# Kernel optimization log

Measured on AMD Instinct MI355X. Metric: run time of the kernel, lower is better.

The kernel has to match this reference:

```python
import jax, jax.numpy as jnp
import numpy as np

SEQ_LEN = 2048
VOCAB = 32000
EMB = 512
HID = 1024


def setup_inputs() -> dict:
    key = jax.random.key(0)
    ks = jax.random.split(key, 8)
    s = lambda n: 1.0 / np.sqrt(n)
    return {
        "tokens": jax.random.randint(ks[0], (SEQ_LEN,), 0, VOCAB, dtype=jnp.int64 if jax.config.jax_enable_x64 else jnp.int32),
        "embedding_mat": jax.random.normal(ks[1], (VOCAB, EMB), dtype=jnp.float32),
        "W1": jax.random.normal(ks[2], (EMB, HID), dtype=jnp.float32) * s(EMB),
        "U1": jax.random.normal(ks[3], (HID, HID), dtype=jnp.float32) * s(HID),
        "b1": jnp.zeros((HID,), dtype=jnp.float32),
        "W2": jax.random.normal(ks[4], (HID, EMB), dtype=jnp.float32) * s(HID),
        "U2": jax.random.normal(ks[5], (EMB, EMB), dtype=jnp.float32) * s(EMB),
        "b2": jnp.zeros((EMB,), dtype=jnp.float32),
    }


def _rnn_scan(inputs, W1, U1, b1, W2, U2, b2):
    # 2-layer vanilla tanh RNN over time; inputs: [T, EMB] -> outputs: [T, EMB]
    h1_0 = jnp.zeros((W1.shape[1],), dtype=inputs.dtype)
    h2_0 = jnp.zeros((W2.shape[1],), dtype=inputs.dtype)

    def step(carry, x_t):
        h1, h2 = carry
        h1 = jnp.tanh(x_t @ W1 + h1 @ U1 + b1)
        h2 = jnp.tanh(h1 @ W2 + h2 @ U2 + b2)
        return (h1, h2), h2

    _, outs = jax.lax.scan(step, (h1_0, h2_0), inputs)
    return outs


def reference(tokens, embedding_mat, W1, U1, b1, W2, U2, b2):
    # embed tokens, shift right by one (teacher forcing with zero BOS)
    embedded = jnp.take(embedding_mat, tokens, axis=0)          # [T, EMB]
    inputs = jnp.pad(embedded, ((1, 0), (0, 0)))[:-1]           # [T, EMB]
    rnn_outputs = _rnn_scan(inputs, W1, U1, b1, W2, U2, b2)     # [T, EMB]
    logits = rnn_outputs @ embedding_mat.T                      # [T, V]
    raw_log_probs = jax.nn.log_softmax(logits, axis=1)          # [T, V]
    log_probs = jnp.take_along_axis(raw_log_probs, tokens[:, None], axis=1)[:, 0]
    return jnp.sum(log_probs)
```

## Files before the change

### kernel.cpp

```cpp
#include <hip/hip_runtime.h>
#include <stdint.h>


#define TSEQ 2048
#define NVOCAB 32000
#define DEMB 512
#define DHID 1024
#define CAN 0xFFFFFFFFu

typedef __attribute__((ext_vector_type(8))) short short8;
typedef __attribute__((ext_vector_type(4))) float f32x4;
typedef unsigned long long u64;

__device__ __forceinline__ unsigned short f2bf(float f) {
  union { float f; unsigned u; } v; v.f = f;
  unsigned r = (v.u + 0x7FFFu + ((v.u >> 16) & 1u)) >> 16;
  return (unsigned short)r;
}

__device__ __forceinline__ f32x4 llc_ld16(const float* p) {
  f32x4 r;
  asm volatile("global_load_dwordx4 %0, %1, off sc0 sc1\n\ts_waitcnt vmcnt(0)"
               : "=&v"(r) : "v"(p) : "memory");
  return r;
}

__device__ __forceinline__ void llc_ld16x2(const float* pa, const float* pb,
                                           f32x4& a, f32x4& b) {
  asm volatile("global_load_dwordx4 %0, %2, off sc0 sc1\n\t"
               "global_load_dwordx4 %1, %3, off sc0 sc1\n\t"
               "s_waitcnt vmcnt(0)"
               : "=&v"(a), "=&v"(b) : "v"(pa), "v"(pb) : "memory");
}

__device__ __forceinline__ void llc_st16(float* p, f32x4 v) {
  asm volatile("global_store_dwordx4 %0, %1, off sc0 sc1"
               :: "v"(p), "v"(v) : "memory");
}

__device__ __forceinline__ bool okq(f32x4 v) {
  return __float_as_uint(v.x) != CAN && __float_as_uint(v.y) != CAN &&
         __float_as_uint(v.z) != CAN && __float_as_uint(v.w) != CAN;
}

__device__ __forceinline__ f32x4 rotq(f32x4 h) {
  f32x4 r;
  r.x = __int_as_float(__builtin_amdgcn_mov_dpp(__float_as_int(h.x), 0x121, 0xf, 0xf, false));
  r.y = __int_as_float(__builtin_amdgcn_mov_dpp(__float_as_int(h.y), 0x121, 0xf, 0xf, false));
  r.z = __int_as_float(__builtin_amdgcn_mov_dpp(__float_as_int(h.z), 0x121, 0xf, 0xf, false));
  r.w = __int_as_float(__builtin_amdgcn_mov_dpp(__float_as_int(h.w), 0x121, 0xf, 0xf, false));
  return r;
}

__device__ __forceinline__ float tanh_fast(float x) {
  float ax = fabsf(x);
  float e = __expf(ax + ax);
  float t = 1.f - __fdividef(2.f, e + 1.f);
  return (x < 0.f) ? -t : t;
}

__global__ void k_init(uint4* __restrict__ h1v4, uint4* __restrict__ h2v4) {
  const int n1 = (TSEQ + 1) * DHID / 4;
  const int n2 = (TSEQ + 1) * DEMB / 4;
  uint4 can; can.x = CAN; can.y = CAN; can.z = CAN; can.w = CAN;
  uint4 zer; zer.x = 0u; zer.y = 0u; zer.z = 0u; zer.w = 0u;
  const int stride = gridDim.x * blockDim.x;
  for (int i = blockIdx.x * blockDim.x + threadIdx.x; i < n1 + n2; i += stride) {
    if (i < n1) {
      h1v4[i] = (i < DHID / 4) ? zer : can;
    } else {
      int j = i - n1;
      h2v4[j] = (j < DEMB / 4) ? zer : can;
    }
  }
}

__global__ __launch_bounds__(256) void k_xw1(const int* __restrict__ tok,
                                             const float* __restrict__ emb,
                                             const float* __restrict__ W1,
                                             const float* __restrict__ b1,
                                             float* __restrict__ xW1) {
  __shared__ float in_lds[16 * DEMB];
  const int tid = threadIdx.x;
  const int rb = blockIdx.x >> 2, cb = blockIdx.x & 3;
  const int t0 = rb * 16, j0 = cb * 256;
  for (int idx = tid; idx < 16 * 128; idx += 256) {
    int r = idx >> 7, q = idx & 127;
    int t = t0 + r;
    float4 v;
    if (t == 0) { v.x = 0.f; v.y = 0.f; v.z = 0.f; v.w = 0.f; }
    else        { v = *(const float4*)(emb + (size_t)tok[t - 1] * DEMB + q * 4); }
    *(float4*)&in_lds[r * DEMB + q * 4] = v;
  }
  __syncthreads();
  const int j = j0 + tid;
  float acc[16];
  {
    float bb = b1[j];
#pragma unroll
    for (int r = 0; r < 16; ++r) acc[r] = bb;
  }
  for (int k = 0; k < DEMB; k += 4) {
    const float* wp = W1 + (size_t)k * DHID + j;
    float w0 = wp[0], w1 = wp[DHID], w2 = wp[2 * DHID], w3 = wp[3 * DHID];
#pragma unroll
    for (int r = 0; r < 16; ++r) {
      float4 h = *(const float4*)&in_lds[r * DEMB + k];
      acc[r] += h.x * w0;
      acc[r] += h.y * w1;
      acc[r] += h.z * w2;
      acc[r] += h.w * w3;
    }
  }
#pragma unroll
  for (int r = 0; r < 16; ++r) xW1[(size_t)(t0 + r) * DHID + j] = acc[r];
}

__global__ __launch_bounds__(256, 1) void k_rnn(const float* __restrict__ xW1,
                                                const float* __restrict__ U1,
                                                const float* __restrict__ W2,
                                                const float* __restrict__ U2,
                                                const float* __restrict__ b2,
                                                float* __restrict__ h1v,
                                                float* __restrict__ h2v,
                                                float* __restrict__ h2buf) {
  __shared__ float cmb[2][160];
  const int tid = threadIdx.x;
  const int wg = blockIdx.x;
  const int l = tid & 63, w = tid >> 6;
  const int r = l >> 4, i = l & 15;

  if (wg < 32) {
    const int c0 = wg * 32;
    float wA[64], wB[64];
#pragma unroll
    for (int j = 0; j < 16; ++j) {
      int sl = (i - j) & 15;
      const float* up = U1 + (size_t)(256 * w + 64 * r + 4 * sl) * DHID + c0;
#pragma unroll
      for (int e = 0; e < 4; ++e) {
        wA[4 * j + e] = up[(size_t)e * DHID + i];
        wB[4 * j + e] = up[(size_t)e * DHID + i + 16];
      }
    }
    for (int st = 0; st < TSEQ; ++st) {
      float xv = 0.f;
      if (w == 0) xv = xW1[(size_t)st * DHID + c0 + (l & 31)];
      f32x4 h;
      {
        const float* sp = h1v + (size_t)st * DHID + 4 * tid;
        while (true) { h = llc_ld16(sp); if (okq(h)) break; }
      }
      float a0 = 0.f, a1 = 0.f;
#pragma unroll
      for (int j = 0; j < 16; ++j) {
        a0 += h.x * wA[4 * j + 0]; a1 += h.x * wB[4 * j + 0];
        a0 += h.y * wA[4 * j + 1]; a1 += h.y * wB[4 * j + 1];
        a0 += h.z * wA[4 * j + 2]; a1 += h.z * wB[4 * j + 2];
        a0 += h.w * wA[4 * j + 3]; a1 += h.w * wB[4 * j + 3];
        if (j < 15) h = rotq(h);
      }
      a0 += __shfl_xor(a0, 16); a0 += __shfl_xor(a0, 32);
      a1 += __shfl_xor(a1, 16); a1 += __shfl_xor(a1, 32);
      const int par = st & 1;
      if (l < 16) {
        cmb[par][i * 5 + w] = a0;
        cmb[par][(i + 16) * 5 + w] = a1;
      }
      __syncthreads();
      if (w == 0) {
        const float* cp = &cmb[par][(l & 31) * 5];
        float s4 = (cp[0] + cp[1]) + (cp[2] + cp[3]);
        float hv = tanh_fast(xv + s4);
        float g1 = __shfl_down(hv, 1);
        float g2 = __shfl_down(hv, 2);
        float g3 = __shfl_down(hv, 3);
        if (l < 32 && (l & 3) == 0) {
          f32x4 o; o.x = hv; o.y = g1; o.z = g2; o.w = g3;
          llc_st16(h1v + (size_t)(st + 1) * DHID + c0 + l, o);
        }
      }
    }
  } else {
    const int c0 = (wg - 32) * 32;
    float qAA[64], qAB[64], qBA[64], qBB[64];
#pragma unroll
    for (int j = 0; j < 16; ++j) {
      int sl = (i - j) & 15;
      const float* mp = W2 + (size_t)(256 * w + 64 * r + 4 * sl) * DEMB + c0;
#pragma unroll
      for (int e = 0; e < 4; ++e) {
        qAA[4 * j + e] = mp[(size_t)e * DEMB + i];
        qAB[4 * j + e] = mp[(size_t)e * DEMB + i + 16];
      }
    }
    if (w < 2) {
#pragma unroll
      for (int j = 0; j < 16; ++j) {
        int sl = (i - j) & 15;
        const float* mp = U2 + (size_t)(256 * w + 64 * r + 4 * sl) * DEMB + c0;
#pragma unroll
        for (int e = 0; e < 4; ++e) {
          qBA[4 * j + e] = mp[(size_t)e * DEMB + i];
          qBB[4 * j + e] = mp[(size_t)e * DEMB + i + 16];
        }
      }
    }
    float bias = 0.f;
    if (w == 0) bias = b2[c0 + (l & 31)];
    for (int t = 0; t < TSEQ; ++t) {
      f32x4 hA, hB;
      const float* spA = h1v + (size_t)(t + 1) * DHID + 4 * tid;
      if (w < 2) {
        const float* spB = h2v + (size_t)t * DEMB + 4 * tid;
        while (true) {
          f32x4 xa, xb;
          llc_ld16x2(spA, spB, xa, xb);
          if (okq(xa) && okq(xb)) { hA = xa; hB = xb; break; }
        }
      } else {
        while (true) { f32x4 xa = llc_ld16(spA); if (okq(xa)) { hA = xa; break; } }
      }
      float a0 = 0.f, a1 = 0.f;
#pragma unroll
      for (int j = 0; j < 16; ++j) {
        a0 += hA.x * qAA[4 * j + 0]; a1 += hA.x * qAB[4 * j + 0];
        a0 += hA.y * qAA[4 * j + 1]; a1 += hA.y * qAB[4 * j + 1];
        a0 += hA.z * qAA[4 * j + 2]; a1 += hA.z * qAB[4 * j + 2];
        a0 += hA.w * qAA[4 * j + 3]; a1 += hA.w * qAB[4 * j + 3];
        if (j < 15) hA = rotq(hA);
      }
      if (w < 2) {
#pragma unroll
        for (int j = 0; j < 16; ++j) {
          a0 += hB.x * qBA[4 * j + 0]; a1 += hB.x * qBB[4 * j + 0];
          a0 += hB.y * qBA[4 * j + 1]; a1 += hB.y * qBB[4 * j + 1];
          a0 += hB.z * qBA[4 * j + 2]; a1 += hB.z * qBB[4 * j + 2];
          a0 += hB.w * qBA[4 * j + 3]; a1 += hB.w * qBB[4 * j + 3];
          if (j < 15) hB = rotq(hB);
        }
      }
      a0 += __shfl_xor(a0, 16); a0 += __shfl_xor(a0, 32);
      a1 += __shfl_xor(a1, 16); a1 += __shfl_xor(a1, 32);
      const int par = t & 1;
      if (l < 16) {
        cmb[par][i * 5 + w] = a0;
        cmb[par][(i + 16) * 5 + w] = a1;
      }
      __syncthreads();
      if (w == 0) {
        const float* cp = &cmb[par][(l & 31) * 5];
        float s4 = (cp[0] + cp[1]) + (cp[2] + cp[3]);
        float hv = tanh_fast(s4 + bias);
        float g1 = __shfl_down(hv, 1);
        float g2 = __shfl_down(hv, 2);
        float g3 = __shfl_down(hv, 3);
        if (l < 32 && (l & 3) == 0) {
          f32x4 o; o.x = hv; o.y = g1; o.z = g2; o.w = g3;
          llc_st16(h2v + (size_t)(t + 1) * DEMB + c0 + l, o);
          *(f32x4*)(h2buf + (size_t)(t + 1) * DEMB + c0 + l) = o;
        }
      }
    }
  }
}

__global__ void k_conv(const float* __restrict__ emb, const float* __restrict__ h2f,
                       unsigned short* __restrict__ embB, unsigned short* __restrict__ h2b) {
  const int n1 = NVOCAB * DEMB / 4;
  const int n2 = TSEQ * DEMB / 4;
  const int stride = gridDim.x * blockDim.x;
  for (int i = blockIdx.x * blockDim.x + threadIdx.x; i < n1 + n2; i += stride) {
    float4 v;
    if (i < n1) v = ((const float4*)emb)[i];
    else        v = ((const float4*)h2f)[i - n1];
    ushort4 o;
    o.x = f2bf(v.x); o.y = f2bf(v.y); o.z = f2bf(v.z); o.w = f2bf(v.w);
    if (i < n1) ((ushort4*)embB)[i] = o;
    else        ((ushort4*)h2b)[i - n1] = o;
  }
}

__global__ __launch_bounds__(256, 1) void k_logits(const unsigned short* __restrict__ Ab,
                                                   const unsigned short* __restrict__ Bb,
                                                   float* __restrict__ pmax,
                                                   float* __restrict__ psum) {
  extern __shared__ char smem_dyn[];
  unsigned short* As = (unsigned short*)smem_dyn;
  float* sstat = (float*)(smem_dyn + 131072);
  const int tid = threadIdx.x;
  const int rb = blockIdx.x >> 4, ch = blockIdx.x & 15;
  const int r0 = rb * 128, v0 = ch * 2000;
  for (int idx = tid; idx < 128 * 64; idx += 256) {
    int row = idx >> 6, kq = idx & 63;
    uint4 v = *(const uint4*)(Ab + (size_t)(r0 + row) * DEMB + kq * 8);
    int byte = (row * 1024 + kq * 16) ^ ((row & 7) << 4);
    *(uint4*)((char*)As + byte) = v;
  }
  __syncthreads();
  const int wv = tid >> 6, lane = tid & 63;
  const int col = lane & 15, kg = lane >> 4;
  f32x4 rmax[8], rsum[8];
#pragma unroll
  for (int t = 0; t < 8; ++t) { rmax[t] = (f32x4)(-3.0e38f); rsum[t] = (f32x4)(0.f); }

  for (int strip = wv; strip < 125; strip += 4) {
    const unsigned short* bp = Bb + (size_t)(v0 + strip * 16 + col) * DEMB + kg * 8;
    f32x4 acc[8];
#pragma unroll
    for (int t = 0; t < 8; ++t) acc[t] = (f32x4)(0.f);
#pragma unroll
    for (int ks = 0; ks < 16; ++ks) {
      short8 bfrag = *(const short8*)(bp + ks * 32);
#pragma unroll
      for (int t = 0; t < 8; ++t) {
        int row = t * 16 + col;
        int byte = (row * 1024 + ks * 64 + kg * 16) ^ ((row & 7) << 4);
        short8 afrag = *(const short8*)((const char*)As + byte);
        acc[t] = __builtin_amdgcn_mfma_f32_16x16x32_bf16(afrag, bfrag, acc[t], 0, 0, 0);
      }
    }
#pragma unroll
    for (int t = 0; t < 8; ++t) {
      f32x4 v = acc[t];
      f32x4 mx = v;
#pragma unroll
      for (int d = 1; d < 16; d <<= 1) {
        mx.x = fmaxf(mx.x, __shfl_xor(mx.x, d));
        mx.y = fmaxf(mx.y, __shfl_xor(mx.y, d));
        mx.z = fmaxf(mx.z, __shfl_xor(mx.z, d));
        mx.w = fmaxf(mx.w, __shfl_xor(mx.w, d));
      }
      f32x4 nm;
      nm.x = fmaxf(rmax[t].x, mx.x);
      nm.y = fmaxf(rmax[t].y, mx.y);
      nm.z = fmaxf(rmax[t].z, mx.z);
      nm.w = fmaxf(rmax[t].w, mx.w);
      f32x4 e;
      e.x = __expf(v.x - nm.x); e.y = __expf(v.y - nm.y);
      e.z = __expf(v.z - nm.z); e.w = __expf(v.w - nm.w);
#pragma unroll
      for (int d = 1; d < 16; d <<= 1) {
        e.x += __shfl_xor(e.x, d);
        e.y += __shfl_xor(e.y, d);
        e.z += __shfl_xor(e.z, d);
        e.w += __shfl_xor(e.w, d);
      }
      rsum[t].x = rsum[t].x * __expf(rmax[t].x - nm.x) + e.x;
      rsum[t].y = rsum[t].y * __expf(rmax[t].y - nm.y) + e.y;
      rsum[t].z = rsum[t].z * __expf(rmax[t].z - nm.z) + e.z;
      rsum[t].w = rsum[t].w * __expf(rmax[t].w - nm.w) + e.w;
      rmax[t] = nm;
    }
  }
  if (col == 0) {
#pragma unroll
    for (int t = 0; t < 8; ++t) {
#pragma unroll
      for (int r = 0; r < 4; ++r) {
        int row = t * 16 + kg * 4 + r;
        sstat[(wv * 128 + row) * 2 + 0] = rmax[t][r];
        sstat[(wv * 128 + row) * 2 + 1] = rsum[t][r];
      }
    }
  }
  __syncthreads();
  if (tid < 128) {
    float m = -3.0e38f, ssum = 0.f;
#pragma unroll
    for (int w2 = 0; w2 < 4; ++w2) {
      float pm = sstat[(w2 * 128 + tid) * 2 + 0];
      float ps = sstat[(w2 * 128 + tid) * 2 + 1];
      float nm2 = fmaxf(m, pm);
      ssum = ssum * __expf(m - nm2) + ps * __expf(pm - nm2);
      m = nm2;
    }
    pmax[(size_t)(r0 + tid) * 16 + ch] = m;
    psum[(size_t)(r0 + tid) * 16 + ch] = ssum;
  }
}

__global__ __launch_bounds__(256) void k_tlogit(const int* __restrict__ tok,
                                                const float* __restrict__ emb,
                                                const float* __restrict__ h2buf,
                                                float* __restrict__ tlog) {
  const int wv = threadIdx.x >> 6, lane = threadIdx.x & 63;
  const int wgid = blockIdx.x * 4 + wv;
  for (int t = wgid; t < TSEQ; t += 128) {
    const float* hp = h2buf + (size_t)(t + 1) * DEMB + lane * 8;
    const float* ep = emb + (size_t)tok[t] * DEMB + lane * 8;
    float4 h0 = *(const float4*)hp, h1v = *(const float4*)(hp + 4);
    float4 e0 = *(const float4*)ep, e1v = *(const float4*)(ep + 4);
    float d = h0.x * e0.x + h0.y * e0.y + h0.z * e0.z + h0.w * e0.w +
              h1v.x * e1v.x + h1v.y * e1v.y + h1v.z * e1v.z + h1v.w * e1v.w;
    for (int m = 1; m < 64; m <<= 1) d += __shfl_xor(d, m);
    if (lane == 0) tlog[t] = d;
  }
}

__global__ void k_final(const float* __restrict__ pmax, const float* __restrict__ psum,
                        const float* __restrict__ tlog, float* __restrict__ out) {
  __shared__ float red[4];
  float local = 0.f;
  for (int t = threadIdx.x; t < TSEQ; t += 256) {
    float m = -3.0e38f, s = 0.f;
#pragma unroll
    for (int c = 0; c < 16; ++c) {
      float pm = pmax[t * 16 + c], ps = psum[t * 16 + c];
      float nm = fmaxf(m, pm);
      s = s * __expf(m - nm) + ps * __expf(pm - nm);
      m = nm;
    }
    local += tlog[t] - (m + __logf(s));
  }
  for (int d = 1; d < 64; d <<= 1) local += __shfl_xor(local, d);
  if ((threadIdx.x & 63) == 0) red[threadIdx.x >> 6] = local;
  __syncthreads();
  if (threadIdx.x == 0) out[0] = red[0] + red[1] + red[2] + red[3];
}

extern "C" void kernel_launch(void* const* d_in, const int* in_sizes, int n_in,
                              void* d_out, int out_size, void* d_ws, size_t ws_size,
                              hipStream_t stream) {
  (void)in_sizes; (void)n_in; (void)out_size; (void)ws_size;
  const int*   tok = (const int*)d_in[0];
  const float* emb = (const float*)d_in[1];
  const float* W1  = (const float*)d_in[2];
  const float* U1  = (const float*)d_in[3];
  const float* b1  = (const float*)d_in[4];
  const float* W2  = (const float*)d_in[5];
  const float* U2  = (const float*)d_in[6];
  const float* b2  = (const float*)d_in[7];
  float* out = (float*)d_out;

  char* ws = (char*)d_ws;
  size_t off = 0;
  auto alloc = [&](size_t bytes) {
    char* p = ws + off;
    off = (off + bytes + 255) & ~(size_t)255;
    return p;
  };
  float* h2buf = (float*)alloc((size_t)(TSEQ + 1) * DEMB * 4);
  unsigned short* h2b = (unsigned short*)alloc((size_t)TSEQ * DEMB * 2);
  float* pmax = (float*)alloc((size_t)TSEQ * 16 * 4);
  float* psum = (float*)alloc((size_t)TSEQ * 16 * 4);
  float* tlog = (float*)alloc((size_t)TSEQ * 4);
  size_t sz_h2v = (size_t)(TSEQ + 1) * DEMB * 4;
  size_t sz_h1v = (size_t)(TSEQ + 1) * DHID * 4;
  size_t sz_xw1 = (size_t)TSEQ * DHID * 4;
  size_t sz_embB = (size_t)NVOCAB * DEMB * 2;
  size_t big_sz = sz_h2v + sz_h1v + sz_xw1;
  if (sz_embB > big_sz) big_sz = sz_embB;
  char* big = alloc(big_sz);
  float* h2v = (float*)big;
  float* h1v = (float*)(big + sz_h2v);
  float* xW1 = (float*)(big + sz_h2v + sz_h1v);
  unsigned short* embB = (unsigned short*)big;

  k_init<<<dim3(512), dim3(256), 0, stream>>>((uint4*)h1v, (uint4*)h2v);
  k_xw1<<<dim3(512), dim3(256), 0, stream>>>(tok, emb, W1, b1, xW1);
  k_rnn<<<dim3(48), dim3(256), 0, stream>>>(xW1, U1, W2, U2, b2, h1v, h2v, h2buf);
  k_conv<<<dim3(2048), dim3(256), 0, stream>>>(emb, h2buf + DEMB, embB, h2b);
  k_logits<<<dim3(256), dim3(256), 135168, stream>>>(h2b, embB, pmax, psum);
  k_tlogit<<<dim3(32), dim3(256), 0, stream>>>(tok, emb, h2buf, tlog);
  k_final<<<dim3(1), dim3(256), 0, stream>>>(pmax, psum, tlog, out);
}
```

Before: 4.392 ms.

## Publish per-wave partial sums instead of block-reduced hidden states in RNN

The recurrent kernel now drops the LDS combine and __syncthreads: each wave writes its partial pre-activation sums straight to a 4-way slotted global buffer. Consumers poll all four partials, then sum them and apply tanh themselves. Layer 2 is re-split into 32 workgroups of 16 columns over a stacked [W2;U2] weight, and the final layer-2 tanh moves into the conversion kernel. This removes a block barrier and a serial tanh/store stage from the per-step critical path, at the cost of 4x polling traffic and redundant tanh work by every consumer.

```diff
diff --git a/kernel.cpp b/kernel.cpp
--- a/kernel.cpp
+++ b/kernel.cpp
@@ -10,6 +10,7 @@
 
 typedef __attribute__((ext_vector_type(8))) short short8;
 typedef __attribute__((ext_vector_type(4))) float f32x4;
+typedef __attribute__((ext_vector_type(2))) float f32x2;
 typedef unsigned long long u64;
 
 __device__ __forceinline__ unsigned short f2bf(float f) {
@@ -18,29 +19,41 @@
   return (unsigned short)r;
 }
 
-__device__ __forceinline__ f32x4 llc_ld16(const float* p) {
-  f32x4 r;
-  asm volatile("global_load_dwordx4 %0, %1, off sc0 sc1\n\ts_waitcnt vmcnt(0)"
-               : "=&v"(r) : "v"(p) : "memory");
-  return r;
-}
-
-__device__ __forceinline__ void llc_ld16x2(const float* pa, const float* pb,
-                                           f32x4& a, f32x4& b) {
-  asm volatile("global_load_dwordx4 %0, %2, off sc0 sc1\n\t"
-               "global_load_dwordx4 %1, %3, off sc0 sc1\n\t"
-               "s_waitcnt vmcnt(0)"
-               : "=&v"(a), "=&v"(b) : "v"(pa), "v"(pb) : "memory");
-}
-
-__device__ __forceinline__ void llc_st16(float* p, f32x4 v) {
-  asm volatile("global_store_dwordx4 %0, %1, off sc0 sc1"
-               :: "v"(p), "v"(v) : "memory");
-}
-
-__device__ __forceinline__ bool okq(f32x4 v) {
-  return __float_as_uint(v.x) != CAN && __float_as_uint(v.y) != CAN &&
-         __float_as_uint(v.z) != CAN && __float_as_uint(v.w) != CAN;
+__device__ __forceinline__ void llc_ld16x4o(const float* p, f32x4& r0, f32x4& r1,
+                                            f32x4& r2, f32x4& r3) {
+  asm volatile(
+      "global_load_dwordx4 %0, %4, off sc0 sc1\n\t"
+      "global_load_dwordx4 %1, %4, off offset:16 sc0 sc1\n\t"
+      "global_load_dwordx4 %2, %4, off offset:32 sc0 sc1\n\t"
+      "global_load_dwordx4 %3, %4, off offset:48 sc0 sc1\n\t"
+      "s_waitcnt vmcnt(0)"
+      : "=&v"(r0), "=&v"(r1), "=&v"(r2), "=&v"(r3)
+      : "v"(p) : "memory");
+}
+
+__device__ __forceinline__ void llc_ld16x6(const float* pa, const float* pb,
+                                           const float* pc, f32x4& a0, f32x4& a1,
+                                           f32x4& b0, f32x4& b1, f32x4& c0,
+                                           f32x4& c1) {
+  asm volatile(
+      "global_load_dwordx4 %0, %6, off sc0 sc1\n\t"
+      "global_load_dwordx4 %1, %6, off offset:16 sc0 sc1\n\t"
+      "global_load_dwordx4 %2, %7, off sc0 sc1\n\t"
+      "global_load_dwordx4 %3, %7, off offset:16 sc0 sc1\n\t"
+      "global_load_dwordx4 %4, %8, off sc0 sc1\n\t"
+      "global_load_dwordx4 %5, %8, off offset:16 sc0 sc1\n\t"
+      "s_waitcnt vmcnt(0)"
+      : "=&v"(a0), "=&v"(a1), "=&v"(b0), "=&v"(b1), "=&v"(c0), "=&v"(c1)
+      : "v"(pa), "v"(pb), "v"(pc) : "memory");
+}
+
+__device__ __forceinline__ void llc_st4(float* p, float v) {
+  asm volatile("global_store_dword %0, %1, off sc0 sc1" :: "v"(p), "v"(v) : "memory");
+}
+
+__device__ __forceinline__ bool okq4(f32x4 v) {
+  return (__float_as_uint(v.x) != CAN) & (__float_as_uint(v.y) != CAN) &
+         (__float_as_uint(v.z) != CAN) & (__float_as_uint(v.w) != CAN);
 }
 
 __device__ __forceinline__ f32x4 rotq(f32x4 h) {
@@ -51,6 +64,12 @@
   r.w = __int_as_float(__builtin_amdgcn_mov_dpp(__float_as_int(h.w), 0x121, 0xf, 0xf, false));
   return r;
 }
+__device__ __forceinline__ f32x2 rotp(f32x2 h) {
+  f32x2 r;
+  r.x = __int_as_float(__builtin_amdgcn_mov_dpp(__float_as_int(h.x), 0x121, 0xf, 0xf, false));
+  r.y = __int_as_float(__builtin_amdgcn_mov_dpp(__float_as_int(h.y), 0x121, 0xf, 0xf, false));
+  return r;
+}
 
 __device__ __forceinline__ float tanh_fast(float x) {
   float ax = fabsf(x);
@@ -59,18 +78,17 @@
   return (x < 0.f) ? -t : t;
 }
 
-__global__ void k_init(uint4* __restrict__ h1v4, uint4* __restrict__ h2v4) {
-  const int n1 = (TSEQ + 1) * DHID / 4;
-  const int n2 = (TSEQ + 1) * DEMB / 4;
+__global__ void k_init(uint4* __restrict__ P1q, uint4* __restrict__ P2q) {
+  const int n1 = (TSEQ + 1) * DHID;
+  const int n2 = (TSEQ + 1) * DEMB;
   uint4 can; can.x = CAN; can.y = CAN; can.z = CAN; can.w = CAN;
   uint4 zer; zer.x = 0u; zer.y = 0u; zer.z = 0u; zer.w = 0u;
   const int stride = gridDim.x * blockDim.x;
   for (int i = blockIdx.x * blockDim.x + threadIdx.x; i < n1 + n2; i += stride) {
-    if (i < n1) {
-      h1v4[i] = (i < DHID / 4) ? zer : can;
-    } else {
+    if (i < n1) P1q[i] = (i < DHID) ? zer : can;
+    else {
       int j = i - n1;
-      h2v4[j] = (j < DEMB / 4) ? zer : can;
+      P2q[j] = (j < DEMB) ? zer : can;
     }
   }
 }
@@ -121,10 +139,8 @@
                                                 const float* __restrict__ W2,
                                                 const float* __restrict__ U2,
                                                 const float* __restrict__ b2,
-                                                float* __restrict__ h1v,
-                                                float* __restrict__ h2v,
-                                                float* __restrict__ h2buf) {
-  __shared__ float cmb[2][160];
+                                                float* __restrict__ P1,
+                                                float* __restrict__ P2) {
   const int tid = threadIdx.x;
   const int wg = blockIdx.x;
   const int l = tid & 63, w = tid >> 6;
@@ -143,14 +159,22 @@
         wB[4 * j + e] = up[(size_t)e * DHID + i + 16];
       }
     }
-    for (int st = 0; st < TSEQ; ++st) {
-      float xv = 0.f;
-      if (w == 0) xv = xW1[(size_t)st * DHID + c0 + (l & 31)];
+    const float* pp = P1 + ((size_t)1 * DHID + 4 * tid) * 4;
+    const float* xp = xW1 + 4 * tid;
+    float* stp = P1 + ((size_t)2 * DHID + c0 + l) * 4 + w;
+    if (l < 32) llc_st4(P1 + ((size_t)1 * DHID + c0 + l) * 4 + w, 0.f);
+    for (int st = 1; st < TSEQ; ++st) {
+      f32x4 xq = *(const f32x4*)xp;
+      f32x4 q0, q1, q2, q3;
+      while (true) {
+        llc_ld16x4o(pp, q0, q1, q2, q3);
+        if (okq4(q0) & okq4(q1) & okq4(q2) & okq4(q3)) break;
+      }
       f32x4 h;
-      {
-        const float* sp = h1v + (size_t)st * DHID + 4 * tid;
-        while (true) { h = llc_ld16(sp); if (okq(h)) break; }
-      }
+      h.x = tanh_fast(xq.x + ((q0.x + q0.y) + (q0.z + q0.w)));
+      h.y = tanh_fast(xq.y + ((q1.x + q1.y) + (q1.z + q1.w)));
+      h.z = tanh_fast(xq.z + ((q2.x + q2.y) + (q2.z + q2.w)));
+      h.w = tanh_fast(xq.w + ((q3.x + q3.y) + (q3.z + q3.w)));
       float a0 = 0.f, a1 = 0.f;
 #pragma unroll
       for (int j = 0; j < 16; ++j) {
@@ -162,122 +186,117 @@
       }
       a0 += __shfl_xor(a0, 16); a0 += __shfl_xor(a0, 32);
       a1 += __shfl_xor(a1, 16); a1 += __shfl_xor(a1, 32);
-      const int par = st & 1;
-      if (l < 16) {
-        cmb[par][i * 5 + w] = a0;
-        cmb[par][(i + 16) * 5 + w] = a1;
-      }
-      __syncthreads();
-      if (w == 0) {
-        const float* cp = &cmb[par][(l & 31) * 5];
-        float s4 = (cp[0] + cp[1]) + (cp[2] + cp[3]);
-        float hv = tanh_fast(xv + s4);
-        float g1 = __shfl_down(hv, 1);
-        float g2 = __shfl_down(hv, 2);
-        float g3 = __shfl_down(hv, 3);
-        if (l < 32 && (l & 3) == 0) {
-          f32x4 o; o.x = hv; o.y = g1; o.z = g2; o.w = g3;
-          llc_st16(h1v + (size_t)(st + 1) * DHID + c0 + l, o);
-        }
-      }
+      if (l < 32) llc_st4(stp, (l < 16) ? a0 : a1);
+      pp += (size_t)DHID * 4;
+      xp += DHID;
+      stp += (size_t)DHID * 4;
     }
   } else {
-    const int c0 = (wg - 32) * 32;
-    float qAA[64], qAB[64], qBA[64], qBB[64];
-#pragma unroll
-    for (int j = 0; j < 16; ++j) {
-      int sl = (i - j) & 15;
-      const float* mp = W2 + (size_t)(256 * w + 64 * r + 4 * sl) * DEMB + c0;
-#pragma unroll
-      for (int e = 0; e < 4; ++e) {
-        qAA[4 * j + e] = mp[(size_t)e * DEMB + i];
-        qAB[4 * j + e] = mp[(size_t)e * DEMB + i + 16];
-      }
-    }
-    if (w < 2) {
+    const int c0 = (wg - 32) * 16;
+    float wm0[32], wm1[32], wm2[32];
+    f32x2 bia0, bia1, bia2;
+    const float *ax0, *ax1, *ax2;
+    const float *sp0, *sp1, *sp2;
+    ptrdiff_t si0, si1, si2;
+    bool z0, z1, z2;
+#define L2SETUP(M, wmM, biaM, axM, spM, siM, zM)                                   \
+    {                                                                              \
+      int kb = 384 * w + 96 * r + 32 * M;                                          \
+      _Pragma("unroll")                                                            \
+      for (int j = 0; j < 16; ++j) {                                               \
+        int kk = kb + 2 * ((i - j) & 15);                                          \
+        const float* m0 = (kk < DHID) ? (W2 + (size_t)kk * DEMB)                   \
+                                      : (U2 + (size_t)(kk - DHID) * DEMB);         \
+        const float* m1 = (kk + 1 < DHID) ? (W2 + (size_t)(kk + 1) * DEMB)         \
+                                          : (U2 + (size_t)(kk + 1 - DHID) * DEMB); \
+        wmM[2 * j] = m0[c0 + i];                                                   \
+        wmM[2 * j + 1] = m1[c0 + i];                                               \
+      }                                                                            \
+      int kr = kb + 2 * i;                                                         \
+      zM = (kr >= DHID);                                                           \
+      int bi = zM ? (kr - DHID) : 0;                                               \
+      biaM.x = b2[bi]; biaM.y = b2[bi + 1];                                        \
+      axM = xW1 + (zM ? (kr & (DHID - 1)) : kr);                                   \
+      spM = zM ? (P2 + ((size_t)(kr - DHID)) * 4)                                  \
+               : (P1 + ((size_t)1 * DHID + kr) * 4);                               \
+      siM = zM ? (ptrdiff_t)(DEMB * 4) : (ptrdiff_t)(DHID * 4);                    \
+    }
+    L2SETUP(0, wm0, bia0, ax0, sp0, si0, z0)
+    L2SETUP(1, wm1, bia1, ax1, sp1, si1, z1)
+    L2SETUP(2, wm2, bia2, ax2, sp2, si2, z2)
+#undef L2SETUP
+    float* stp = P2 + ((size_t)1 * DEMB + c0 + (l & 15)) * 4 + w;
+    for (int t = 0; t < TSEQ; ++t) {
+      f32x2 x0 = *(const f32x2*)ax0;
+      f32x2 x1 = *(const f32x2*)ax1;
+      f32x2 x2 = *(const f32x2*)ax2;
+      f32x4 A0, A1, B0, B1, C0, C1;
+      while (true) {
+        llc_ld16x6(sp0, sp1, sp2, A0, A1, B0, B1, C0, C1);
+        if (okq4(A0) & okq4(A1) & okq4(B0) & okq4(B1) & okq4(C0) & okq4(C1)) break;
+      }
+      f32x2 v0 = z0 ? bia0 : x0;
+      f32x2 v1 = z1 ? bia1 : x1;
+      f32x2 v2 = z2 ? bia2 : x2;
+      const bool zz = (t == 0);
+      f32x2 hA, hB, hC;
+      hA.x = (zz & z0) ? 0.f : tanh_fast(v0.x + ((A0.x + A0.y) + (A0.z + A0.w)));
+      hA.y = (zz & z0) ? 0.f : tanh_fast(v0.y + ((A1.x + A1.y) + (A1.z + A1.w)));
+      hB.x = (zz & z1) ? 0.f : tanh_fast(v1.x + ((B0.x + B0.y) + (B0.z + B0.w)));
+      hB.y = (zz & z1) ? 0.f : tanh_fast(v1.y + ((B1.x + B1.y) + (B1.z + B1.w)));
+      hC.x = (zz & z2) ? 0.f : tanh_fast(v2.x + ((C0.x + C0.y) + (C0.z + C0.w)));
+      hC.y = (zz & z2) ? 0.f : tanh_fast(v2.y + ((C1.x + C1.y) + (C1.z + C1.w)));
+      float a0 = 0.f, a1 = 0.f, a2 = 0.f;
 #pragma unroll
       for (int j = 0; j < 16; ++j) {
-        int sl = (i - j) & 15;
-        const float* mp = U2 + (size_t)(256 * w + 64 * r + 4 * sl) * DEMB + c0;
-#pragma unroll
-        for (int e = 0; e < 4; ++e) {
-          qBA[4 * j + e] = mp[(size_t)e * DEMB + i];
-          qBB[4 * j + e] = mp[(size_t)e * DEMB + i + 16];
-        }
-      }
-    }
-    float bias = 0.f;
-    if (w == 0) bias = b2[c0 + (l & 31)];
-    for (int t = 0; t < TSEQ; ++t) {
-      f32x4 hA, hB;
-      const float* spA = h1v + (size_t)(t + 1) * DHID + 4 * tid;
-      if (w < 2) {
-        const float* spB = h2v + (size_t)t * DEMB + 4 * tid;
-        while (true) {
-          f32x4 xa, xb;
-          llc_ld16x2(spA, spB, xa, xb);
-          if (okq(xa) && okq(xb)) { hA = xa; hB = xb; break; }
-        }
-      } else {
-        while (true) { f32x4 xa = llc_ld16(spA); if (okq(xa)) { hA = xa; break; } }
-      }
-      float a0 = 0.f, a1 = 0.f;
-#pragma unroll
-      for (int j = 0; j < 16; ++j) {
-        a0 += hA.x * qAA[4 * j + 0]; a1 += hA.x * qAB[4 * j + 0];
-        a0 += hA.y * qAA[4 * j + 1]; a1 += hA.y * qAB[4 * j + 1];
-        a0 += hA.z * qAA[4 * j + 2]; a1 += hA.z * qAB[4 * j + 2];
-        a0 += hA.w * qAA[4 * j + 3]; a1 += hA.w * qAB[4 * j + 3];
-        if (j < 15) hA = rotq(hA);
-      }
-      if (w < 2) {
-#pragma unroll
-        for (int j = 0; j < 16; ++j) {
-          a0 += hB.x * qBA[4 * j + 0]; a1 += hB.x * qBB[4 * j + 0];
-          a0 += hB.y * qBA[4 * j + 1]; a1 += hB.y * qBB[4 * j + 1];
-          a0 += hB.z * qBA[4 * j + 2]; a1 += hB.z * qBB[4 * j + 2];
-          a0 += hB.w * qBA[4 * j + 3]; a1 += hB.w * qBB[4 * j + 3];
-          if (j < 15) hB = rotq(hB);
-        }
-      }
-      a0 += __shfl_xor(a0, 16); a0 += __shfl_xor(a0, 32);
-      a1 += __shfl_xor(a1, 16); a1 += __shfl_xor(a1, 32);
-      const int par = t & 1;
-      if (l < 16) {
-        cmb[par][i * 5 + w] = a0;
-        cmb[par][(i + 16) * 5 + w] = a1;
-      }
-      __syncthreads();
-      if (w == 0) {
-        const float* cp = &cmb[par][(l & 31) * 5];
-        float s4 = (cp[0] + cp[1]) + (cp[2] + cp[3]);
-        float hv = tanh_fast(s4 + bias);
-        float g1 = __shfl_down(hv, 1);
-        float g2 = __shfl_down(hv, 2);
-        float g3 = __shfl_down(hv, 3);
-        if (l < 32 && (l & 3) == 0) {
-          f32x4 o; o.x = hv; o.y = g1; o.z = g2; o.w = g3;
-          llc_st16(h2v + (size_t)(t + 1) * DEMB + c0 + l, o);
-          *(f32x4*)(h2buf + (size_t)(t + 1) * DEMB + c0 + l) = o;
-        }
-      }
-    }
-  }
-}
-
-__global__ void k_conv(const float* __restrict__ emb, const float* __restrict__ h2f,
-                       unsigned short* __restrict__ embB, unsigned short* __restrict__ h2b) {
+        a0 += hA.x * wm0[2 * j]; a0 += hA.y * wm0[2 * j + 1];
+        a1 += hB.x * wm1[2 * j]; a1 += hB.y * wm1[2 * j + 1];
+        a2 += hC.x * wm2[2 * j]; a2 += hC.y * wm2[2 * j + 1];
+        if (j < 15) { hA = rotp(hA); hB = rotp(hB); hC = rotp(hC); }
+      }
+      float a = (a0 + a1) + a2;
+      a += __shfl_xor(a, 16); a += __shfl_xor(a, 32);
+      if (l < 16) llc_st4(stp, a);
+      sp0 += si0; sp1 += si1; sp2 += si2;
+      ax0 += DHID; ax1 += DHID; ax2 += DHID;
+      stp += (size_t)DEMB * 4;
+    }
+  }
+}
+
+__global__ void k_conv(const float* __restrict__ emb, const float* __restrict__ P2,
+                       const float* __restrict__ b2,
+                       unsigned short* __restrict__ embB,
+                       unsigned short* __restrict__ h2b, float* __restrict__ h2buf) {
   const int n1 = NVOCAB * DEMB / 4;
   const int n2 = TSEQ * DEMB / 4;
   const int stride = gridDim.x * blockDim.x;
-  for (int i = blockIdx.x * blockDim.x + threadIdx.x; i < n1 + n2; i += stride) {
-    float4 v;
-    if (i < n1) v = ((const float4*)emb)[i];
-    else        v = ((const float4*)h2f)[i - n1];
-    ushort4 o;
-    o.x = f2bf(v.x); o.y = f2bf(v.y); o.z = f2bf(v.z); o.w = f2bf(v.w);
-    if (i < n1) ((ushort4*)embB)[i] = o;
-    else        ((ushort4*)h2b)[i - n1] = o;
+  for (int idx = blockIdx.x * blockDim.x + threadIdx.x; idx < n1 + n2; idx += stride) {
+    if (idx < n1) {
+      float4 v = ((const float4*)emb)[idx];
+      ushort4 o;
+      o.x = f2bf(v.x); o.y = f2bf(v.y); o.z = f2bf(v.z); o.w = f2bf(v.w);
+      ((ushort4*)embB)[idx] = o;
+    } else {
+      int j = idx - n1;
+      int s = 1 + (j >> 7);
+      int q = (j & 127) << 2;
+      const float* pb = P2 + ((size_t)s * DEMB + q) * 4;
+      float4 A = *(const float4*)pb;
+      float4 B = *(const float4*)(pb + 4);
+      float4 C = *(const float4*)(pb + 8);
+      float4 D = *(const float4*)(pb + 12);
+      float4 bq = *(const float4*)(b2 + q);
+      float4 h;
+      h.x = tanh_fast(bq.x + ((A.x + A.y) + (A.z + A.w)));
+      h.y = tanh_fast(bq.y + ((B.x + B.y) + (B.z + B.w)));
+      h.z = tanh_fast(bq.z + ((C.x + C.y) + (C.z + C.w)));
+      h.w = tanh_fast(bq.w + ((D.x + D.y) + (D.z + D.w)));
+      *(float4*)(h2buf + (size_t)s * DEMB + q) = h;
+      ushort4 o;
+      o.x = f2bf(h.x); o.y = f2bf(h.y); o.z = f2bf(h.z); o.w = f2bf(h.w);
+      ((ushort4*)h2b)[((size_t)(s - 1) * DEMB + q) >> 2] = o;
+    }
   }
 }
 
@@ -445,22 +464,22 @@
   float* pmax = (float*)alloc((size_t)TSEQ * 16 * 4);
   float* psum = (float*)alloc((size_t)TSEQ * 16 * 4);
   float* tlog = (float*)alloc((size_t)TSEQ * 4);
-  size_t sz_h2v = (size_t)(TSEQ + 1) * DEMB * 4;
-  size_t sz_h1v = (size_t)(TSEQ + 1) * DHID * 4;
+  size_t sz_P1 = (size_t)(TSEQ + 1) * DHID * 4 * 4;
   size_t sz_xw1 = (size_t)TSEQ * DHID * 4;
+  size_t sz_P2 = (size_t)(TSEQ + 1) * DEMB * 4 * 4;
   size_t sz_embB = (size_t)NVOCAB * DEMB * 2;
-  size_t big_sz = sz_h2v + sz_h1v + sz_xw1;
+  size_t big_sz = sz_P1 + sz_xw1 + sz_P2;
   if (sz_embB > big_sz) big_sz = sz_embB;
   char* big = alloc(big_sz);
-  float* h2v = (float*)big;
-  float* h1v = (float*)(big + sz_h2v);
-  float* xW1 = (float*)(big + sz_h2v + sz_h1v);
+  float* P1 = (float*)big;
+  float* xW1 = (float*)(big + sz_P1);
+  float* P2 = (float*)(big + sz_P1 + sz_xw1);
   unsigned short* embB = (unsigned short*)big;
 
-  k_init<<<dim3(512), dim3(256), 0, stream>>>((uint4*)h1v, (uint4*)h2v);
+  k_init<<<dim3(512), dim3(256), 0, stream>>>((uint4*)P1, (uint4*)P2);
   k_xw1<<<dim3(512), dim3(256), 0, stream>>>(tok, emb, W1, b1, xW1);
-  k_rnn<<<dim3(48), dim3(256), 0, stream>>>(xW1, U1, W2, U2, b2, h1v, h2v, h2buf);
-  k_conv<<<dim3(2048), dim3(256), 0, stream>>>(emb, h2buf + DEMB, embB, h2b);
+  k_rnn<<<dim3(64), dim3(256), 0, stream>>>(xW1, U1, W2, U2, b2, P1, P2);
+  k_conv<<<dim3(2048), dim3(256), 0, stream>>>(emb, P2, b2, embB, h2b, h2buf);
   k_logits<<<dim3(256), dim3(256), 135168, stream>>>(h2b, embB, pmax, psum);
   k_tlogit<<<dim3(32), dim3(256), 0, stream>>>(tok, emb, h2buf, tlog);
   k_final<<<dim3(1), dim3(256), 0, stream>>>(pmax, psum, tlog, out);
```

Result: slower. 7.357 ms (+67.5%).

## Split persistent RNN across twice as many workgroups with 16 columns each

Applied to the files above, without the earlier changes.

Doubles the persistent RNN grid from 48 to 96 workgroups, so each handles 16 output columns instead of 32. Layer 2's U2 work is now spread over all four waves with half-width loads instead of two waves doing double work. The per-step serial chain gets shorter: half the FMAs per thread, one accumulator split into four independent lanes, and scalar stores from 16 threads instead of shuffle-packed vector stores. The trade-off is more workgroups polling the shared flag-based buffers each step, which raises cross-CU synchronization traffic.

```diff
diff --git a/kernel.cpp b/kernel.cpp
--- a/kernel.cpp
+++ b/kernel.cpp
@@ -10,6 +10,7 @@
 
 typedef __attribute__((ext_vector_type(8))) short short8;
 typedef __attribute__((ext_vector_type(4))) float f32x4;
+typedef __attribute__((ext_vector_type(2))) float f32x2;
 typedef unsigned long long u64;
 
 __device__ __forceinline__ unsigned short f2bf(float f) {
@@ -25,22 +26,24 @@
   return r;
 }
 
-__device__ __forceinline__ void llc_ld16x2(const float* pa, const float* pb,
-                                           f32x4& a, f32x4& b) {
+__device__ __forceinline__ void llc_ld16_8(const float* pa, const float* pb,
+                                           f32x4& a, f32x2& b) {
   asm volatile("global_load_dwordx4 %0, %2, off sc0 sc1\n\t"
-               "global_load_dwordx4 %1, %3, off sc0 sc1\n\t"
+               "global_load_dwordx2 %1, %3, off sc0 sc1\n\t"
                "s_waitcnt vmcnt(0)"
                : "=&v"(a), "=&v"(b) : "v"(pa), "v"(pb) : "memory");
 }
 
-__device__ __forceinline__ void llc_st16(float* p, f32x4 v) {
-  asm volatile("global_store_dwordx4 %0, %1, off sc0 sc1"
-               :: "v"(p), "v"(v) : "memory");
-}
-
-__device__ __forceinline__ bool okq(f32x4 v) {
-  return __float_as_uint(v.x) != CAN && __float_as_uint(v.y) != CAN &&
-         __float_as_uint(v.z) != CAN && __float_as_uint(v.w) != CAN;
+__device__ __forceinline__ void llc_st4(float* p, float v) {
+  asm volatile("global_store_dword %0, %1, off sc0 sc1" :: "v"(p), "v"(v) : "memory");
+}
+
+__device__ __forceinline__ bool okq4(f32x4 v) {
+  return (__float_as_uint(v.x) != CAN) & (__float_as_uint(v.y) != CAN) &
+         (__float_as_uint(v.z) != CAN) & (__float_as_uint(v.w) != CAN);
+}
+__device__ __forceinline__ bool okp2(f32x2 v) {
+  return (__float_as_uint(v.x) != CAN) & (__float_as_uint(v.y) != CAN);
 }
 
 __device__ __forceinline__ f32x4 rotq(f32x4 h) {
@@ -49,6 +52,12 @@
   r.y = __int_as_float(__builtin_amdgcn_mov_dpp(__float_as_int(h.y), 0x121, 0xf, 0xf, false));
   r.z = __int_as_float(__builtin_amdgcn_mov_dpp(__float_as_int(h.z), 0x121, 0xf, 0xf, false));
   r.w = __int_as_float(__builtin_amdgcn_mov_dpp(__float_as_int(h.w), 0x121, 0xf, 0xf, false));
+  return r;
+}
+__device__ __forceinline__ f32x2 rotp(f32x2 h) {
+  f32x2 r;
+  r.x = __int_as_float(__builtin_amdgcn_mov_dpp(__float_as_int(h.x), 0x121, 0xf, 0xf, false));
+  r.y = __int_as_float(__builtin_amdgcn_mov_dpp(__float_as_int(h.y), 0x121, 0xf, 0xf, false));
   return r;
 }
 
@@ -124,143 +133,100 @@
                                                 float* __restrict__ h1v,
                                                 float* __restrict__ h2v,
                                                 float* __restrict__ h2buf) {
-  __shared__ float cmb[2][160];
+  __shared__ float cmb[2][128];
   const int tid = threadIdx.x;
   const int wg = blockIdx.x;
   const int l = tid & 63, w = tid >> 6;
   const int r = l >> 4, i = l & 15;
 
-  if (wg < 32) {
-    const int c0 = wg * 32;
-    float wA[64], wB[64];
+  if (wg < 64) {
+    const int c0 = wg * 16;
+    float wA[64];
 #pragma unroll
     for (int j = 0; j < 16; ++j) {
       int sl = (i - j) & 15;
-      const float* up = U1 + (size_t)(256 * w + 64 * r + 4 * sl) * DHID + c0;
-#pragma unroll
-      for (int e = 0; e < 4; ++e) {
-        wA[4 * j + e] = up[(size_t)e * DHID + i];
-        wB[4 * j + e] = up[(size_t)e * DHID + i + 16];
-      }
-    }
+      const float* up = U1 + (size_t)(256 * w + 64 * r + 4 * sl) * DHID + c0 + i;
+#pragma unroll
+      for (int e = 0; e < 4; ++e) wA[4 * j + e] = up[(size_t)e * DHID];
+    }
+    const float* pp = h1v + 4 * tid;
+    const float* xp = xW1 + c0 + (tid & 15);
+    float* stp = h1v + DHID + c0 + tid;
     for (int st = 0; st < TSEQ; ++st) {
-      float xv = 0.f;
-      if (w == 0) xv = xW1[(size_t)st * DHID + c0 + (l & 31)];
+      float xv = *xp;
       f32x4 h;
-      {
-        const float* sp = h1v + (size_t)st * DHID + 4 * tid;
-        while (true) { h = llc_ld16(sp); if (okq(h)) break; }
-      }
-      float a0 = 0.f, a1 = 0.f;
+      while (true) { h = llc_ld16(pp); if (okq4(h)) break; }
+      f32x4 ac = (f32x4)(0.f);
 #pragma unroll
       for (int j = 0; j < 16; ++j) {
-        a0 += h.x * wA[4 * j + 0]; a1 += h.x * wB[4 * j + 0];
-        a0 += h.y * wA[4 * j + 1]; a1 += h.y * wB[4 * j + 1];
-        a0 += h.z * wA[4 * j + 2]; a1 += h.z * wB[4 * j + 2];
-        a0 += h.w * wA[4 * j + 3]; a1 += h.w * wB[4 * j + 3];
+        ac.x += h.x * wA[4 * j + 0];
+        ac.y += h.y * wA[4 * j + 1];
+        ac.z += h.z * wA[4 * j + 2];
+        ac.w += h.w * wA[4 * j + 3];
         if (j < 15) h = rotq(h);
       }
-      a0 += __shfl_xor(a0, 16); a0 += __shfl_xor(a0, 32);
-      a1 += __shfl_xor(a1, 16); a1 += __shfl_xor(a1, 32);
+      float a = (ac.x + ac.y) + (ac.z + ac.w);
+      a += __shfl_xor(a, 16);
+      a += __shfl_xor(a, 32);
       const int par = st & 1;
-      if (l < 16) {
-        cmb[par][i * 5 + w] = a0;
-        cmb[par][(i + 16) * 5 + w] = a1;
-      }
+      if (l < 16) cmb[par][i * 8 + w] = a;
       __syncthreads();
-      if (w == 0) {
-        const float* cp = &cmb[par][(l & 31) * 5];
-        float s4 = (cp[0] + cp[1]) + (cp[2] + cp[3]);
-        float hv = tanh_fast(xv + s4);
-        float g1 = __shfl_down(hv, 1);
-        float g2 = __shfl_down(hv, 2);
-        float g3 = __shfl_down(hv, 3);
-        if (l < 32 && (l & 3) == 0) {
-          f32x4 o; o.x = hv; o.y = g1; o.z = g2; o.w = g3;
-          llc_st16(h1v + (size_t)(st + 1) * DHID + c0 + l, o);
-        }
-      }
+      if (tid < 16) {
+        f32x4 c4 = *(const f32x4*)&cmb[par][tid * 8];
+        float hv = tanh_fast(xv + ((c4.x + c4.y) + (c4.z + c4.w)));
+        llc_st4(stp, hv);
+      }
+      pp += DHID; xp += DHID; stp += DHID;
     }
   } else {
-    const int c0 = (wg - 32) * 32;
-    float qAA[64], qAB[64], qBA[64], qBB[64];
+    const int c0 = (wg - 64) * 16;
+    float wq[64], wp[32];
 #pragma unroll
     for (int j = 0; j < 16; ++j) {
       int sl = (i - j) & 15;
-      const float* mp = W2 + (size_t)(256 * w + 64 * r + 4 * sl) * DEMB + c0;
-#pragma unroll
-      for (int e = 0; e < 4; ++e) {
-        qAA[4 * j + e] = mp[(size_t)e * DEMB + i];
-        qAB[4 * j + e] = mp[(size_t)e * DEMB + i + 16];
-      }
-    }
-    if (w < 2) {
+      const float* m = W2 + (size_t)(256 * w + 64 * r + 4 * sl) * DEMB + c0 + i;
+#pragma unroll
+      for (int e = 0; e < 4; ++e) wq[4 * j + e] = m[(size_t)e * DEMB];
+      const float* u = U2 + (size_t)(128 * w + 32 * r + 2 * sl) * DEMB + c0 + i;
+      wp[2 * j + 0] = u[0];
+      wp[2 * j + 1] = u[DEMB];
+    }
+    const float bias = b2[c0 + (tid & 15)];
+    const float* ppA = h1v + DHID + 256 * w + 64 * r + 4 * i;
+    const float* ppB = h2v + 128 * w + 32 * r + 2 * i;
+    float* stp = h2v + DEMB + c0 + tid;
+    float* hb = h2buf + DEMB + c0 + tid;
+    for (int t = 0; t < TSEQ; ++t) {
+      f32x4 hq; f32x2 hp;
+      while (true) {
+        llc_ld16_8(ppA, ppB, hq, hp);
+        if (okq4(hq) & okp2(hp)) break;
+      }
+      f32x4 aq = (f32x4)(0.f);
+      f32x2 ap = (f32x2)(0.f);
 #pragma unroll
       for (int j = 0; j < 16; ++j) {
-        int sl = (i - j) & 15;
-        const float* mp = U2 + (size_t)(256 * w + 64 * r + 4 * sl) * DEMB + c0;
-#pragma unroll
-        for (int e = 0; e < 4; ++e) {
-          qBA[4 * j + e] = mp[(size_t)e * DEMB + i];
-          qBB[4 * j + e] = mp[(size_t)e * DEMB + i + 16];
-        }
-      }
-    }
-    float bias = 0.f;
-    if (w == 0) bias = b2[c0 + (l & 31)];
-    for (int t = 0; t < TSEQ; ++t) {
-      f32x4 hA, hB;
-      const float* spA = h1v + (size_t)(t + 1) * DHID + 4 * tid;
-      if (w < 2) {
-        const float* spB = h2v + (size_t)t * DEMB + 4 * tid;
-        while (true) {
-          f32x4 xa, xb;
-          llc_ld16x2(spA, spB, xa, xb);
-          if (okq(xa) && okq(xb)) { hA = xa; hB = xb; break; }
-        }
-      } else {
-        while (true) { f32x4 xa = llc_ld16(spA); if (okq(xa)) { hA = xa; break; } }
-      }
-      float a0 = 0.f, a1 = 0.f;
-#pragma unroll
-      for (int j = 0; j < 16; ++j) {
-        a0 += hA.x * qAA[4 * j + 0]; a1 += hA.x * qAB[4 * j + 0];
-        a0 += hA.y * qAA[4 * j + 1]; a1 += hA.y * qAB[4 * j + 1];
-        a0 += hA.z * qAA[4 * j + 2]; a1 += hA.z * qAB[4 * j + 2];
-        a0 += hA.w * qAA[4 * j + 3]; a1 += hA.w * qAB[4 * j + 3];
-        if (j < 15) hA = rotq(hA);
-      }
-      if (w < 2) {
-#pragma unroll
-        for (int j = 0; j < 16; ++j) {
-          a0 += hB.x * qBA[4 * j + 0]; a1 += hB.x * qBB[4 * j + 0];
-          a0 += hB.y * qBA[4 * j + 1]; a1 += hB.y * qBB[4 * j + 1];
-          a0 += hB.z * qBA[4 * j + 2]; a1 += hB.z * qBB[4 * j + 2];
-          a0 += hB.w * qBA[4 * j + 3]; a1 += hB.w * qBB[4 * j + 3];
-          if (j < 15) hB = rotq(hB);
-        }
-      }
-      a0 += __shfl_xor(a0, 16); a0 += __shfl_xor(a0, 32);
-      a1 += __shfl_xor(a1, 16); a1 += __shfl_xor(a1, 32);
+        aq.x += hq.x * wq[4 * j + 0];
+        aq.y += hq.y * wq[4 * j + 1];
+        aq.z += hq.z * wq[4 * j + 2];
+        aq.w += hq.w * wq[4 * j + 3];
+        ap.x += hp.x * wp[2 * j + 0];
+        ap.y += hp.y * wp[2 * j + 1];
+        if (j < 15) { hq = rotq(hq); hp = rotp(hp); }
+      }
+      float a = ((aq.x + aq.y) + (aq.z + aq.w)) + (ap.x + ap.y);
+      a += __shfl_xor(a, 16);
+      a += __shfl_xor(a, 32);
       const int par = t & 1;
-      if (l < 16) {
-        cmb[par][i * 5 + w] = a0;
-        cmb[par][(i + 16) * 5 + w] = a1;
-      }
+      if (l < 16) cmb[par][i * 8 + w] = a;
       __syncthreads();
-      if (w == 0) {
-        const float* cp = &cmb[par][(l & 31) * 5];
-        float s4 = (cp[0] + cp[1]) + (cp[2] + cp[3]);
-        float hv = tanh_fast(s4 + bias);
-        float g1 = __shfl_down(hv, 1);
-        float g2 = __shfl_down(hv, 2);
-        float g3 = __shfl_down(hv, 3);
-        if (l < 32 && (l & 3) == 0) {
-          f32x4 o; o.x = hv; o.y = g1; o.z = g2; o.w = g3;
-          llc_st16(h2v + (size_t)(t + 1) * DEMB + c0 + l, o);
-          *(f32x4*)(h2buf + (size_t)(t + 1) * DEMB + c0 + l) = o;
-        }
-      }
+      if (tid < 16) {
+        f32x4 c4 = *(const f32x4*)&cmb[par][tid * 8];
+        float hv = tanh_fast(bias + ((c4.x + c4.y) + (c4.z + c4.w)));
+        llc_st4(stp, hv);
+        *hb = hv;
+      }
+      ppA += DHID; ppB += DEMB; stp += DEMB; hb += DEMB;
     }
   }
 }
@@ -459,7 +425,7 @@
 
   k_init<<<dim3(512), dim3(256), 0, stream>>>((uint4*)h1v, (uint4*)h2v);
   k_xw1<<<dim3(512), dim3(256), 0, stream>>>(tok, emb, W1, b1, xW1);
-  k_rnn<<<dim3(48), dim3(256), 0, stream>>>(xW1, U1, W2, U2, b2, h1v, h2v, h2buf);
+  k_rnn<<<dim3(96), dim3(256), 0, stream>>>(xW1, U1, W2, U2, b2, h1v, h2v, h2buf);
   k_conv<<<dim3(2048), dim3(256), 0, stream>>>(emb, h2buf + DEMB, embB, h2b);
   k_logits<<<dim3(256), dim3(256), 135168, stream>>>(h2b, embB, pmax, psum);
   k_tlogit<<<dim3(32), dim3(256), 0, stream>>>(tok, emb, h2buf, tlog);
```

New measurement: 3.810 ms. 13.2% less time.
